# Kernel optimization log

Hardware: AMD Instinct MI355X
Metric: run time of the kernel (lower is better)

Reference implementation:

```python
import jax, jax.numpy as jnp
import numpy as np

HEADS = 8
DIM_HEAD = 32
SCALE = DIM_HEAD ** -0.5


def _split_heads(t):
    # [b, n, h*d] -> [b, h, n, d]
    b, n, hd = t.shape
    return t.reshape(b, n, HEADS, hd // HEADS).transpose(0, 2, 1, 3)


def setup_inputs() -> dict:
    key = jax.random.key(0)
    k1, k2, k3, k4 = jax.random.split(key, 4)
    b, n, dim = 2, 2048, 256
    inner = HEADS * DIM_HEAD  # 256
    x = jax.random.normal(k1, (b, n, dim), dtype=jnp.float32)
    attn_feat = jax.random.normal(k2, (b, n, dim), dtype=jnp.float32)
    # nn.Linear(dim, 3*inner, bias=False): store as [dim, 3*inner] for x @ W
    W_qkv = jax.random.normal(k3, (dim, 3 * inner), dtype=jnp.float32) * (dim ** -0.5)
    W_qkv_aux = jax.random.normal(k4, (dim, 3 * inner), dtype=jnp.float32) * (dim ** -0.5)
    return {"x": x, "attn_feat": attn_feat, "W_qkv": W_qkv, "W_qkv_aux": W_qkv_aux,
            "use_cls_tokens": 1}


def reference(x, attn_feat, W_qkv, W_qkv_aux, use_cls_tokens):
    b, n, dim = x.shape
    # aux Q,K (v_aux computed but unused, matching original chunk of 3)
    qkv_aux = attn_feat @ W_qkv_aux            # [b, n, 3*inner]
    q_aux, k_aux, _ = jnp.split(qkv_aux, 3, axis=-1)
    q_aux, k_aux = _split_heads(q_aux), _split_heads(k_aux)
    # self Q,K
    qkv_self = x @ W_qkv
    q_self, k_self, _ = jnp.split(qkv_self, 3, axis=-1)
    q_self, k_self = _split_heads(q_self), _split_heads(k_self)
    # dual score product: (QK^T_aux * scale) * (QK^T_self * scale)
    dots_aux = jnp.einsum('bhid,bhjd->bhij', q_aux, k_aux) * SCALE
    dots_self = jnp.einsum('bhid,bhjd->bhij', q_self, k_self) * SCALE
    attn = jax.nn.softmax(dots_aux * dots_self, axis=-1)  # [b, h, n, n]
    # v = x.unsqueeze(1): broadcast raw x over heads
    out = jnp.einsum('bhij,bjd->bhid', attn, x)           # [b, h, n, dim]
    out = out.transpose(0, 2, 1, 3).reshape(b, n, HEADS * dim)
    attn_flat = attn.transpose(0, 2, 1, 3).reshape(b, n, HEADS * n)
    return (out, out[:, 0], attn_flat[:, 0])
```

## Files before the change

kernel.cpp:

```cpp
#include <hip/hip_runtime.h>

typedef _Float16 f16;
typedef _Float16 f16x4 __attribute__((ext_vector_type(4)));
typedef _Float16 f16x8 __attribute__((ext_vector_type(8)));
typedef float f32x4 __attribute__((ext_vector_type(4)));

#define LOG2E 1.4426950408889634f
#define SCL   (1.4426950408889634f / 32.0f)
#define TH_RAW 177.445f

__global__ __launch_bounds__(256) void k_transpose(const float* __restrict__ x,
                                                   f16* __restrict__ xt) {
  __shared__ f16 tile[64][65];
  int n0 = blockIdx.x * 64;
  int d0 = blockIdx.y * 64;
  int b  = blockIdx.z;
  int t = threadIdx.x;
  int colr = t & 63, rowg = t >> 6;
#pragma unroll
  for (int r = 0; r < 16; ++r) {
    int row = r * 4 + rowg;
    tile[row][colr] = (f16)x[((size_t)b * 2048 + n0 + row) * 256 + d0 + colr];
  }
  __syncthreads();
#pragma unroll
  for (int r = 0; r < 16; ++r) {
    int drow = r * 4 + rowg;
    xt[((size_t)b * 256 + d0 + drow) * 2048 + n0 + colr] = tile[colr][drow];
  }
}

__global__ __launch_bounds__(256) void k_transW(const float* __restrict__ Wq,
    const float* __restrict__ Wa, f16* __restrict__ Wt) {
  __shared__ f16 tile[64][65];
  int n0 = blockIdx.x * 64, k0 = blockIdx.y * 64, s = blockIdx.z;
  const float* W = s ? Wa : Wq;
  f16* dst = Wt + (size_t)s * 512 * 256;
  int t = threadIdx.x, c = t & 63, rg = t >> 6;
#pragma unroll
  for (int r = 0; r < 16; ++r) {
    int krow = r * 4 + rg;
    tile[krow][c] = (f16)W[(size_t)(k0 + krow) * 768 + n0 + c];
  }
  __syncthreads();
#pragma unroll
  for (int r = 0; r < 16; ++r) {
    int nrow = r * 4 + rg;
    dst[(size_t)(n0 + nrow) * 256 + k0 + c] = tile[c][nrow];
  }
}

__global__ __launch_bounds__(256) void k_proj(const float* __restrict__ x,
    const float* __restrict__ af, const f16* __restrict__ Wt,
    f16* __restrict__ Qs, f16* __restrict__ Ks,
    f16* __restrict__ Qa, f16* __restrict__ Ka) {
  int mt = blockIdx.x, nt = blockIdx.y, s = blockIdx.z;
  const float* A = s ? af : x;
  const f16* W = Wt + (size_t)s * 512 * 256;
  f16* Qd = s ? Qa : Qs;
  f16* Kd = s ? Ka : Ks;
  int t = threadIdx.x, wv = t >> 6, ln = t & 63, cl = ln & 15, g = ln >> 4;
  int m0 = mt * 64, n0 = nt * 64;
  const float* arow = A + (size_t)(m0 + wv * 16 + cl) * 256 + g * 8;
  const f16* wb = W + (size_t)n0 * 256 + g * 8;
  f32x4 z4 = {0.f, 0.f, 0.f, 0.f};
  f32x4 acc[4] = {z4, z4, z4, z4};
#pragma unroll
  for (int k32 = 0; k32 < 8; ++k32) {
    float4 u = *(const float4*)(arow + k32 * 32);
    float4 v = *(const float4*)(arow + k32 * 32 + 4);
    f16x8 a = { (f16)u.x, (f16)u.y, (f16)u.z, (f16)u.w,
                (f16)v.x, (f16)v.y, (f16)v.z, (f16)v.w };
#pragma unroll
    for (int n4 = 0; n4 < 4; ++n4) {
      f16x8 bf = *(const f16x8*)(wb + (size_t)(n4 * 16 + cl) * 256 + k32 * 32);
      acc[n4] = __builtin_amdgcn_mfma_f32_16x16x32_f16(a, bf, acc[n4], 0, 0, 0);
    }
  }
#pragma unroll
  for (int n4 = 0; n4 < 4; ++n4) {
    int c = n0 + n4 * 16 + cl;
    int head = (c & 255) >> 5, d = c & 31;
    f16* dst = (c < 256) ? Qd : Kd;
#pragma unroll
    for (int r = 0; r < 4; ++r) {
      int m = m0 + wv * 16 + g * 4 + r;
      int bb = m >> 11, nn = m & 2047;
      dst[(((size_t)bb * 8 + head) * 2048 + nn) * 32 + d] = (f16)acc[n4][r];
    }
  }
}

__global__ __launch_bounds__(256, 2) void k_flash(const f16* __restrict__ Qs,
    const f16* __restrict__ Ks, const f16* __restrict__ Qa,
    const f16* __restrict__ Ka, const f16* __restrict__ xt,
    float* __restrict__ out, float* __restrict__ out_cls) {
  __shared__ f16 KaL[2][64][40];
  __shared__ f16 KsL[2][64][40];
  __shared__ f16 PL[2][64][72];
  __shared__ float alphaL[2][64] __attribute__((aligned(16)));
  __shared__ int   rsF[2][4] __attribute__((aligned(16)));
  __shared__ float lL[64];
  int qt = blockIdx.x, h = blockIdx.y, b = blockIdx.z;
  int bh = b * 8 + h;
  int t = threadIdx.x, wv = t >> 6, ln = t & 63, cl = ln & 15, g = ln >> 4;
  int qrow0 = qt * 64 + wv * 16;
  f16x8 qsf = *(const f16x8*)&Qs[((size_t)bh * 2048 + qrow0 + cl) * 32 + g * 8];
  f16x8 qaf = *(const f16x8*)&Qa[((size_t)bh * 2048 + qrow0 + cl) * 32 + g * 8];
  f32x4 z4 = {0.f, 0.f, 0.f, 0.f};
  f32x4 acc[4][4];
#pragma unroll
  for (int i = 0; i < 4; ++i)
#pragma unroll
    for (int j = 0; j < 4; ++j) acc[i][j] = z4;
  float m_run = -3.0e38f, l_run = 0.f;
  int krow = t >> 2, koff = (t & 3) * 8;
  const f16* kaSrc = Ka + ((size_t)bh * 2048 + krow) * 32 + koff;
  const f16* ksSrc = Ks + ((size_t)bh * 2048 + krow) * 32 + koff;
  const f16* xb = xt + ((size_t)b * 256 + wv * 64) * 2048;

  float tv[16];
  f16x8 xf[2][4];

  auto SCORE_MM = [&](int buf) {
#pragma unroll
    for (int jt = 0; jt < 4; ++jt) {
      f16x8 kaf = *(const f16x8*)&KaL[buf][jt * 16 + cl][g * 8];
      f16x8 ksf = *(const f16x8*)&KsL[buf][jt * 16 + cl][g * 8];
      f32x4 za = __builtin_amdgcn_mfma_f32_16x16x32_f16(kaf, qaf, z4, 0, 0, 0);
      f32x4 zs = __builtin_amdgcn_mfma_f32_16x16x32_f16(ksf, qsf, z4, 0, 0, 0);
#pragma unroll
      for (int r = 0; r < 4; ++r) tv[jt * 4 + r] = za[r] * zs[r];
    }
  };

  auto SCORE_FIN = [&](int buf) {
    float a0 = fmaxf(tv[0], tv[1]),   a1 = fmaxf(tv[2], tv[3]);
    float a2 = fmaxf(tv[4], tv[5]),   a3 = fmaxf(tv[6], tv[7]);
    float a4 = fmaxf(tv[8], tv[9]),   a5 = fmaxf(tv[10], tv[11]);
    float a6 = fmaxf(tv[12], tv[13]), a7 = fmaxf(tv[14], tv[15]);
    float b0 = fmaxf(a0, a1), b1 = fmaxf(a2, a3);
    float b2 = fmaxf(a4, a5), b3 = fmaxf(a6, a7);
    float tm = fmaxf(fmaxf(b0, b1), fmaxf(b2, b3));
    tm = fmaxf(tm, __shfl_xor(tm, 16, 64));
    tm = fmaxf(tm, __shfl_xor(tm, 32, 64));
    bool upd = tm > m_run + TH_RAW;
    float m_new = upd ? tm : m_run;
    float alpha = upd ? exp2f((m_run - m_new) * SCL) : 1.0f;
    float mS = m_new * SCL;
    float p[16];
#pragma unroll
    for (int i = 0; i < 16; ++i) p[i] = exp2f(fmaf(tv[i], SCL, -mS));
    float s0 = p[0] + p[1],   s1 = p[2] + p[3];
    float s2 = p[4] + p[5],   s3 = p[6] + p[7];
    float s4 = p[8] + p[9],   s5 = p[10] + p[11];
    float s6 = p[12] + p[13], s7 = p[14] + p[15];
    float u0 = s0 + s1, u1 = s2 + s3, u2 = s4 + s5, u3 = s6 + s7;
    float ls = (u0 + u1) + (u2 + u3);
    ls += __shfl_xor(ls, 16, 64);
    ls += __shfl_xor(ls, 32, 64);
    l_run = fmaf(l_run, alpha, ls);
    m_run = m_new;
#pragma unroll
    for (int jt = 0; jt < 4; ++jt) {
      auto lo = __builtin_amdgcn_cvt_pkrtz(p[jt * 4 + 0], p[jt * 4 + 1]);
      auto hi = __builtin_amdgcn_cvt_pkrtz(p[jt * 4 + 2], p[jt * 4 + 3]);
      f16x4 pk = { (f16)lo[0], (f16)lo[1], (f16)hi[0], (f16)hi[1] };
      *(f16x4*)&PL[buf][wv * 16 + cl][jt * 16 + g * 4] = pk;
    }
    if (g == 0) alphaL[buf][wv * 16 + cl] = alpha;
    int wany = __any(upd) ? 1 : 0;
    if (ln == 0) rsF[buf][wv] = wany;
  };

  auto XFLOAD = [&](int kt) {
#pragma unroll
    for (int ks2 = 0; ks2 < 2; ++ks2)
#pragma unroll
      for (int ddt = 0; ddt < 4; ++ddt)
        xf[ks2][ddt] = *(const f16x8*)(xb + (size_t)(ddt * 16 + cl) * 2048 +
                                       kt * 64 + ks2 * 32 + g * 8);
  };

  auto PVDO = [&](int pbuf) {
    int4 fl = *(const int4*)&rsF[pbuf][0];
    int flq[4] = { fl.x, fl.y, fl.z, fl.w };
#pragma unroll
    for (int qt2 = 0; qt2 < 4; ++qt2) {
      if (flq[qt2]) {
        f32x4 a4 = *(const f32x4*)&alphaL[pbuf][qt2 * 16 + g * 4];
#pragma unroll
        for (int ddt = 0; ddt < 4; ++ddt)
#pragma unroll
          for (int r = 0; r < 4; ++r) acc[qt2][ddt][r] *= a4[r];
      }
    }
#pragma unroll
    for (int ks2 = 0; ks2 < 2; ++ks2) {
      f16x8 pf[4];
#pragma unroll
      for (int qt2 = 0; qt2 < 4; ++qt2)
        pf[qt2] = *(const f16x8*)&PL[pbuf][qt2 * 16 + cl][ks2 * 32 + g * 8];
#pragma unroll
      for (int ddt = 0; ddt < 4; ++ddt)
#pragma unroll
        for (int qt2 = 0; qt2 < 4; ++qt2)
          acc[qt2][ddt] = __builtin_amdgcn_mfma_f32_16x16x32_f16(
              pf[qt2], xf[ks2][ddt], acc[qt2][ddt], 0, 0, 0);
    }
  };

  *(f16x8*)&KaL[0][krow][koff] = *(const f16x8*)kaSrc;
  *(f16x8*)&KsL[0][krow][koff] = *(const f16x8*)ksSrc;
  __syncthreads();

  f16x8 kan = *(const f16x8*)(kaSrc + 2048);
  f16x8 ksn = *(const f16x8*)(ksSrc + 2048);
  SCORE_MM(0);
  SCORE_FIN(0);
  *(f16x8*)&KaL[1][krow][koff] = kan;
  *(f16x8*)&KsL[1][krow][koff] = ksn;
  __syncthreads();

  for (int k = 1; k < 32; ++k) {
    int sbuf = k & 1, pbuf = sbuf ^ 1;
    XFLOAD(k - 1);
    if (k < 31) {
      kan = *(const f16x8*)(kaSrc + (size_t)(k + 1) * 2048);
      ksn = *(const f16x8*)(ksSrc + (size_t)(k + 1) * 2048);
    }
    SCORE_MM(sbuf);
    PVDO(pbuf);
    SCORE_FIN(sbuf);
    if (k < 31) {
      *(f16x8*)&KaL[pbuf][krow][koff] = kan;
      *(f16x8*)&KsL[pbuf][krow][koff] = ksn;
    }
    __syncthreads();
  }

  XFLOAD(31);
  PVDO(1);

  if (g == 0) lL[wv * 16 + cl] = l_run;
  __syncthreads();
#pragma unroll
  for (int qt2 = 0; qt2 < 4; ++qt2) {
#pragma unroll
    for (int r = 0; r < 4; ++r) {
      float linv = 1.0f / lL[qt2 * 16 + g * 4 + r];
      int q = qt * 64 + qt2 * 16 + g * 4 + r;
#pragma unroll
      for (int ddt = 0; ddt < 4; ++ddt) {
        float v = acc[qt2][ddt][r] * linv;
        int col = h * 256 + wv * 64 + ddt * 16 + cl;
        out[((size_t)b * 2048 + q) * 2048 + col] = v;
        if (q == 0) out_cls[(size_t)b * 2048 + col] = v;
      }
    }
  }
}

__global__ __launch_bounds__(256) void k_attn0(const f16* __restrict__ Qs,
    const f16* __restrict__ Ks, const f16* __restrict__ Qa,
    const f16* __restrict__ Ka, float* __restrict__ dst) {
  __shared__ float qa_s[32], qs_s[32];
  __shared__ float red[256];
  int h = blockIdx.x, b = blockIdx.y, bh = b * 8 + h;
  int t = threadIdx.x;
  if (t < 32) {
    qa_s[t] = (float)Qa[(size_t)bh * 2048 * 32 + t];
    qs_s[t] = (float)Qs[(size_t)bh * 2048 * 32 + t];
  }
  __syncthreads();
  float sv[8];
#pragma unroll
  for (int r = 0; r < 8; ++r) {
    int j = r * 256 + t;
    const f16x8* ka8 = (const f16x8*)&Ka[((size_t)bh * 2048 + j) * 32];
    const f16x8* ks8 = (const f16x8*)&Ks[((size_t)bh * 2048 + j) * 32];
    float da = 0.f, ds = 0.f;
#pragma unroll
    for (int c = 0; c < 4; ++c) {
      f16x8 va = ka8[c], vs = ks8[c];
#pragma unroll
      for (int d = 0; d < 8; ++d) {
        da += qa_s[c * 8 + d] * (float)va[d];
        ds += qs_s[c * 8 + d] * (float)vs[d];
      }
    }
    sv[r] = da * ds * (1.f / 32.f);
  }
  float mx = sv[0];
#pragma unroll
  for (int r = 1; r < 8; ++r) mx = fmaxf(mx, sv[r]);
  red[t] = mx;
  __syncthreads();
  for (int st = 128; st > 0; st >>= 1) {
    if (t < st) red[t] = fmaxf(red[t], red[t + st]);
    __syncthreads();
  }
  float m = red[0];
  __syncthreads();
  float e[8], sum = 0.f;
#pragma unroll
  for (int r = 0; r < 8; ++r) {
    e[r] = exp2f((sv[r] - m) * LOG2E);
    sum += e[r];
  }
  red[t] = sum;
  __syncthreads();
  for (int st = 128; st > 0; st >>= 1) {
    if (t < st) red[t] += red[t + st];
    __syncthreads();
  }
  float l = red[0];
#pragma unroll
  for (int r = 0; r < 8; ++r)
    dst[(size_t)b * 16384 + h * 2048 + r * 256 + t] = e[r] / l;
}

extern "C" void kernel_launch(void* const* d_in, const int* in_sizes, int n_in,
                              void* d_out, int out_size, void* d_ws, size_t ws_size,
                              hipStream_t stream) {
  const float* x  = (const float*)d_in[0];
  const float* af = (const float*)d_in[1];
  const float* Wq = (const float*)d_in[2];
  const float* Wa = (const float*)d_in[3];
  const size_t QK = (size_t)2 * 8 * 2048 * 32;
  f16* Qs = (f16*)d_ws;
  f16* Ks = Qs + QK;
  f16* Qa = Ks + QK;
  f16* Ka = Qa + QK;
  f16* xt = Ka + QK;
  f16* Wt = xt + QK;
  float* out     = (float*)d_out;
  float* out_cls = out + (size_t)2 * 2048 * 2048;
  float* attn0   = out_cls + 2 * 2048;

  k_transpose<<<dim3(32, 4, 2), 256, 0, stream>>>(x, xt);
  k_transW<<<dim3(8, 4, 2), 256, 0, stream>>>(Wq, Wa, Wt);
  k_proj<<<dim3(64, 8, 2), 256, 0, stream>>>(x, af, Wt, Qs, Ks, Qa, Ka);
  k_flash<<<dim3(32, 8, 2), 256, 0, stream>>>(Qs, Ks, Qa, Ka, xt, out, out_cls);
  k_attn0<<<dim3(8, 2), 256, 0, stream>>>(Qs, Ks, Qa, Ka, attn0);
}
```

Measured before the change: 178.4 us.

## Load K tiles straight into registers and skip redundant softmax max reductions

```diff
diff --git a/kernel.cpp b/kernel.cpp
--- a/kernel.cpp
+++ b/kernel.cpp
@@ -95,8 +95,6 @@
     const f16* __restrict__ Ks, const f16* __restrict__ Qa,
     const f16* __restrict__ Ka, const f16* __restrict__ xt,
     float* __restrict__ out, float* __restrict__ out_cls) {
-  __shared__ f16 KaL[2][64][40];
-  __shared__ f16 KsL[2][64][40];
   __shared__ f16 PL[2][64][72];
   __shared__ float alphaL[2][64] __attribute__((aligned(16)));
   __shared__ int   rsF[2][4] __attribute__((aligned(16)));
@@ -113,22 +111,28 @@
   for (int i = 0; i < 4; ++i)
 #pragma unroll
     for (int j = 0; j < 4; ++j) acc[i][j] = z4;
-  float m_run = -3.0e38f, l_run = 0.f;
-  int krow = t >> 2, koff = (t & 3) * 8;
-  const f16* kaSrc = Ka + ((size_t)bh * 2048 + krow) * 32 + koff;
-  const f16* ksSrc = Ks + ((size_t)bh * 2048 + krow) * 32 + koff;
+  float m_run = -3.0e38f, l_lane = 0.f;
+  const f16* kaBase = Ka + ((size_t)bh * 2048 + cl) * 32 + g * 8;
+  const f16* ksBase = Ks + ((size_t)bh * 2048 + cl) * 32 + g * 8;
   const f16* xb = xt + ((size_t)b * 256 + wv * 64) * 2048;
 
   float tv[16];
   f16x8 xf[2][4];
-
-  auto SCORE_MM = [&](int buf) {
+  f16x8 kaA[4], ksA[4], kaB[4], ksB[4];
+
+  auto LOADK = [&](int kt, f16x8 (&ka)[4], f16x8 (&ks)[4]) {
 #pragma unroll
     for (int jt = 0; jt < 4; ++jt) {
-      f16x8 kaf = *(const f16x8*)&KaL[buf][jt * 16 + cl][g * 8];
-      f16x8 ksf = *(const f16x8*)&KsL[buf][jt * 16 + cl][g * 8];
-      f32x4 za = __builtin_amdgcn_mfma_f32_16x16x32_f16(kaf, qaf, z4, 0, 0, 0);
-      f32x4 zs = __builtin_amdgcn_mfma_f32_16x16x32_f16(ksf, qsf, z4, 0, 0, 0);
+      ka[jt] = *(const f16x8*)(kaBase + (size_t)(kt * 64 + jt * 16) * 32);
+      ks[jt] = *(const f16x8*)(ksBase + (size_t)(kt * 64 + jt * 16) * 32);
+    }
+  };
+
+  auto SCORE_MM = [&](f16x8 (&ka)[4], f16x8 (&ks)[4]) {
+#pragma unroll
+    for (int jt = 0; jt < 4; ++jt) {
+      f32x4 za = __builtin_amdgcn_mfma_f32_16x16x32_f16(ka[jt], qaf, z4, 0, 0, 0);
+      f32x4 zs = __builtin_amdgcn_mfma_f32_16x16x32_f16(ks[jt], qsf, z4, 0, 0, 0);
 #pragma unroll
       for (int r = 0; r < 4; ++r) tv[jt * 4 + r] = za[r] * zs[r];
     }
@@ -141,13 +145,19 @@
     float a6 = fmaxf(tv[12], tv[13]), a7 = fmaxf(tv[14], tv[15]);
     float b0 = fmaxf(a0, a1), b1 = fmaxf(a2, a3);
     float b2 = fmaxf(a4, a5), b3 = fmaxf(a6, a7);
-    float tm = fmaxf(fmaxf(b0, b1), fmaxf(b2, b3));
-    tm = fmaxf(tm, __shfl_xor(tm, 16, 64));
-    tm = fmaxf(tm, __shfl_xor(tm, 32, 64));
-    bool upd = tm > m_run + TH_RAW;
-    float m_new = upd ? tm : m_run;
-    float alpha = upd ? exp2f((m_run - m_new) * SCL) : 1.0f;
-    float mS = m_new * SCL;
+    float lmax = fmaxf(fmaxf(b0, b1), fmaxf(b2, b3));
+    int wflag = 0;
+    if (__any(lmax > m_run + TH_RAW)) {
+      float tm = fmaxf(lmax, __shfl_xor(lmax, 16, 64));
+      tm = fmaxf(tm, __shfl_xor(tm, 32, 64));
+      float m_new = fmaxf(m_run, tm);
+      float alpha = exp2f((m_run - m_new) * SCL);
+      l_lane *= alpha;
+      m_run = m_new;
+      if (g == 0) alphaL[buf][wv * 16 + cl] = alpha;
+      wflag = 1;
+    }
+    float mS = m_run * SCL;
     float p[16];
 #pragma unroll
     for (int i = 0; i < 16; ++i) p[i] = exp2f(fmaf(tv[i], SCL, -mS));
@@ -156,11 +166,7 @@
     float s4 = p[8] + p[9],   s5 = p[10] + p[11];
     float s6 = p[12] + p[13], s7 = p[14] + p[15];
     float u0 = s0 + s1, u1 = s2 + s3, u2 = s4 + s5, u3 = s6 + s7;
-    float ls = (u0 + u1) + (u2 + u3);
-    ls += __shfl_xor(ls, 16, 64);
-    ls += __shfl_xor(ls, 32, 64);
-    l_run = fmaf(l_run, alpha, ls);
-    m_run = m_new;
+    l_lane += (u0 + u1) + (u2 + u3);
 #pragma unroll
     for (int jt = 0; jt < 4; ++jt) {
       auto lo = __builtin_amdgcn_cvt_pkrtz(p[jt * 4 + 0], p[jt * 4 + 1]);
@@ -168,9 +174,7 @@
       f16x4 pk = { (f16)lo[0], (f16)lo[1], (f16)hi[0], (f16)hi[1] };
       *(f16x4*)&PL[buf][wv * 16 + cl][jt * 16 + g * 4] = pk;
     }
-    if (g == 0) alphaL[buf][wv * 16 + cl] = alpha;
-    int wany = __any(upd) ? 1 : 0;
-    if (ln == 0) rsF[buf][wv] = wany;
+    if (ln == 0) rsF[buf][wv] = wflag;
   };
 
   auto XFLOAD = [&](int kt) {
@@ -210,39 +214,39 @@
     }
   };
 
-  *(f16x8*)&KaL[0][krow][koff] = *(const f16x8*)kaSrc;
-  *(f16x8*)&KsL[0][krow][koff] = *(const f16x8*)ksSrc;
-  __syncthreads();
-
-  f16x8 kan = *(const f16x8*)(kaSrc + 2048);
-  f16x8 ksn = *(const f16x8*)(ksSrc + 2048);
-  SCORE_MM(0);
+  LOADK(0, kaA, ksA);
+  LOADK(1, kaB, ksB);
+  SCORE_MM(kaA, ksA);
   SCORE_FIN(0);
-  *(f16x8*)&KaL[1][krow][koff] = kan;
-  *(f16x8*)&KsL[1][krow][koff] = ksn;
-  __syncthreads();
-
-  for (int k = 1; k < 32; ++k) {
-    int sbuf = k & 1, pbuf = sbuf ^ 1;
+  __syncthreads();
+
+  for (int k2 = 0; k2 < 15; ++k2) {
+    int k = 2 * k2 + 1;
     XFLOAD(k - 1);
-    if (k < 31) {
-      kan = *(const f16x8*)(kaSrc + (size_t)(k + 1) * 2048);
-      ksn = *(const f16x8*)(ksSrc + (size_t)(k + 1) * 2048);
-    }
-    SCORE_MM(sbuf);
-    PVDO(pbuf);
-    SCORE_FIN(sbuf);
-    if (k < 31) {
-      *(f16x8*)&KaL[pbuf][krow][koff] = kan;
-      *(f16x8*)&KsL[pbuf][krow][koff] = ksn;
-    }
+    LOADK(k + 1, kaA, ksA);
+    SCORE_MM(kaB, ksB);
+    PVDO(0);
+    SCORE_FIN(1);
     __syncthreads();
-  }
-
+    XFLOAD(k);
+    LOADK(k + 2, kaB, ksB);
+    SCORE_MM(kaA, ksA);
+    PVDO(1);
+    SCORE_FIN(0);
+    __syncthreads();
+  }
+
+  XFLOAD(30);
+  SCORE_MM(kaB, ksB);
+  PVDO(0);
+  SCORE_FIN(1);
+  __syncthreads();
   XFLOAD(31);
   PVDO(1);
 
-  if (g == 0) lL[wv * 16 + cl] = l_run;
+  l_lane += __shfl_xor(l_lane, 16, 64);
+  l_lane += __shfl_xor(l_lane, 32, 64);
+  if (g == 0) lL[wv * 16 + cl] = l_lane;
   __syncthreads();
 #pragma unroll
   for (int qt2 = 0; qt2 < 4; ++qt2) {
```

New measurement: 211.8 us. +18.7%, slower.

## Split flash output dim across two blocks and defer row-sum reduction

Applied to the files above, without the earlier changes.

```diff
diff --git a/kernel.cpp b/kernel.cpp
--- a/kernel.cpp
+++ b/kernel.cpp
@@ -91,7 +91,7 @@
   }
 }
 
-__global__ __launch_bounds__(256, 2) void k_flash(const f16* __restrict__ Qs,
+__global__ __launch_bounds__(256, 4) void k_flash(const f16* __restrict__ Qs,
     const f16* __restrict__ Ks, const f16* __restrict__ Qa,
     const f16* __restrict__ Ka, const f16* __restrict__ xt,
     float* __restrict__ out, float* __restrict__ out_cls) {
@@ -101,26 +101,27 @@
   __shared__ float alphaL[2][64] __attribute__((aligned(16)));
   __shared__ int   rsF[2][4] __attribute__((aligned(16)));
   __shared__ float lL[64];
-  int qt = blockIdx.x, h = blockIdx.y, b = blockIdx.z;
+  int qt = blockIdx.x >> 1, ddh = blockIdx.x & 1;
+  int h = blockIdx.y, b = blockIdx.z;
   int bh = b * 8 + h;
   int t = threadIdx.x, wv = t >> 6, ln = t & 63, cl = ln & 15, g = ln >> 4;
   int qrow0 = qt * 64 + wv * 16;
   f16x8 qsf = *(const f16x8*)&Qs[((size_t)bh * 2048 + qrow0 + cl) * 32 + g * 8];
   f16x8 qaf = *(const f16x8*)&Qa[((size_t)bh * 2048 + qrow0 + cl) * 32 + g * 8];
   f32x4 z4 = {0.f, 0.f, 0.f, 0.f};
-  f32x4 acc[4][4];
+  f32x4 acc[4][2];
 #pragma unroll
   for (int i = 0; i < 4; ++i)
 #pragma unroll
-    for (int j = 0; j < 4; ++j) acc[i][j] = z4;
-  float m_run = -3.0e38f, l_run = 0.f;
+    for (int j = 0; j < 2; ++j) acc[i][j] = z4;
+  float m_run = -3.0e38f, l_lane = 0.f;
   int krow = t >> 2, koff = (t & 3) * 8;
   const f16* kaSrc = Ka + ((size_t)bh * 2048 + krow) * 32 + koff;
   const f16* ksSrc = Ks + ((size_t)bh * 2048 + krow) * 32 + koff;
-  const f16* xb = xt + ((size_t)b * 256 + wv * 64) * 2048;
+  const f16* xb = xt + ((size_t)b * 256 + ddh * 128 + wv * 32) * 2048;
 
   float tv[16];
-  f16x8 xf[2][4];
+  f16x8 xf[2][2];
 
   auto SCORE_MM = [&](int buf) {
 #pragma unroll
@@ -141,13 +142,19 @@
     float a6 = fmaxf(tv[12], tv[13]), a7 = fmaxf(tv[14], tv[15]);
     float b0 = fmaxf(a0, a1), b1 = fmaxf(a2, a3);
     float b2 = fmaxf(a4, a5), b3 = fmaxf(a6, a7);
-    float tm = fmaxf(fmaxf(b0, b1), fmaxf(b2, b3));
-    tm = fmaxf(tm, __shfl_xor(tm, 16, 64));
-    tm = fmaxf(tm, __shfl_xor(tm, 32, 64));
-    bool upd = tm > m_run + TH_RAW;
-    float m_new = upd ? tm : m_run;
-    float alpha = upd ? exp2f((m_run - m_new) * SCL) : 1.0f;
-    float mS = m_new * SCL;
+    float lmax = fmaxf(fmaxf(b0, b1), fmaxf(b2, b3));
+    int wflag = 0;
+    if (__any(lmax > m_run + TH_RAW)) {
+      float tm = fmaxf(lmax, __shfl_xor(lmax, 16, 64));
+      tm = fmaxf(tm, __shfl_xor(tm, 32, 64));
+      float m_new = fmaxf(m_run, tm);
+      float alpha = exp2f((m_run - m_new) * SCL);
+      l_lane *= alpha;
+      m_run = m_new;
+      if (g == 0) alphaL[buf][wv * 16 + cl] = alpha;
+      wflag = 1;
+    }
+    float mS = m_run * SCL;
     float p[16];
 #pragma unroll
     for (int i = 0; i < 16; ++i) p[i] = exp2f(fmaf(tv[i], SCL, -mS));
@@ -156,11 +163,7 @@
     float s4 = p[8] + p[9],   s5 = p[10] + p[11];
     float s6 = p[12] + p[13], s7 = p[14] + p[15];
     float u0 = s0 + s1, u1 = s2 + s3, u2 = s4 + s5, u3 = s6 + s7;
-    float ls = (u0 + u1) + (u2 + u3);
-    ls += __shfl_xor(ls, 16, 64);
-    ls += __shfl_xor(ls, 32, 64);
-    l_run = fmaf(l_run, alpha, ls);
-    m_run = m_new;
+    l_lane += (u0 + u1) + (u2 + u3);
 #pragma unroll
     for (int jt = 0; jt < 4; ++jt) {
       auto lo = __builtin_amdgcn_cvt_pkrtz(p[jt * 4 + 0], p[jt * 4 + 1]);
@@ -168,16 +171,14 @@
       f16x4 pk = { (f16)lo[0], (f16)lo[1], (f16)hi[0], (f16)hi[1] };
       *(f16x4*)&PL[buf][wv * 16 + cl][jt * 16 + g * 4] = pk;
     }
-    if (g == 0) alphaL[buf][wv * 16 + cl] = alpha;
-    int wany = __any(upd) ? 1 : 0;
-    if (ln == 0) rsF[buf][wv] = wany;
+    if (ln == 0) rsF[buf][wv] = wflag;
   };
 
   auto XFLOAD = [&](int kt) {
 #pragma unroll
     for (int ks2 = 0; ks2 < 2; ++ks2)
 #pragma unroll
-      for (int ddt = 0; ddt < 4; ++ddt)
+      for (int ddt = 0; ddt < 2; ++ddt)
         xf[ks2][ddt] = *(const f16x8*)(xb + (size_t)(ddt * 16 + cl) * 2048 +
                                        kt * 64 + ks2 * 32 + g * 8);
   };
@@ -190,7 +191,7 @@
       if (flq[qt2]) {
         f32x4 a4 = *(const f32x4*)&alphaL[pbuf][qt2 * 16 + g * 4];
 #pragma unroll
-        for (int ddt = 0; ddt < 4; ++ddt)
+        for (int ddt = 0; ddt < 2; ++ddt)
 #pragma unroll
           for (int r = 0; r < 4; ++r) acc[qt2][ddt][r] *= a4[r];
       }
@@ -202,7 +203,7 @@
       for (int qt2 = 0; qt2 < 4; ++qt2)
         pf[qt2] = *(const f16x8*)&PL[pbuf][qt2 * 16 + cl][ks2 * 32 + g * 8];
 #pragma unroll
-      for (int ddt = 0; ddt < 4; ++ddt)
+      for (int ddt = 0; ddt < 2; ++ddt)
 #pragma unroll
         for (int qt2 = 0; qt2 < 4; ++qt2)
           acc[qt2][ddt] = __builtin_amdgcn_mfma_f32_16x16x32_f16(
@@ -242,7 +243,9 @@
   XFLOAD(31);
   PVDO(1);
 
-  if (g == 0) lL[wv * 16 + cl] = l_run;
+  l_lane += __shfl_xor(l_lane, 16, 64);
+  l_lane += __shfl_xor(l_lane, 32, 64);
+  if (g == 0) lL[wv * 16 + cl] = l_lane;
   __syncthreads();
 #pragma unroll
   for (int qt2 = 0; qt2 < 4; ++qt2) {
@@ -251,9 +254,9 @@
       float linv = 1.0f / lL[qt2 * 16 + g * 4 + r];
       int q = qt * 64 + qt2 * 16 + g * 4 + r;
 #pragma unroll
-      for (int ddt = 0; ddt < 4; ++ddt) {
+      for (int ddt = 0; ddt < 2; ++ddt) {
         float v = acc[qt2][ddt][r] * linv;
-        int col = h * 256 + wv * 64 + ddt * 16 + cl;
+        int col = h * 256 + ddh * 128 + wv * 32 + ddt * 16 + cl;
         out[((size_t)b * 2048 + q) * 2048 + col] = v;
         if (q == 0) out_cls[(size_t)b * 2048 + col] = v;
       }
@@ -341,6 +344,6 @@
   k_transpose<<<dim3(32, 4, 2), 256, 0, stream>>>(x, xt);
   k_transW<<<dim3(8, 4, 2), 256, 0, stream>>>(Wq, Wa, Wt);
   k_proj<<<dim3(64, 8, 2), 256, 0, stream>>>(x, af, Wt, Qs, Ks, Qa, Ka);
-  k_flash<<<dim3(32, 8, 2), 256, 0, stream>>>(Qs, Ks, Qa, Ka, xt, out, out_cls);
+  k_flash<<<dim3(64, 8, 2), 256, 0, stream>>>(Qs, Ks, Qa, Ka, xt, out, out_cls);
   k_attn0<<<dim3(8, 2), 256, 0, stream>>>(Qs, Ks, Qa, Ka, attn0);
 }
```

Measured after the change: 194.7 us. 1.09x slower.
